# Kernel optimization log

Measured on AMD Instinct MI355X. Metric: run time of the kernel, lower is better.

The kernel has to match this reference:

```python
import jax, jax.numpy as jnp
import numpy as np

H, D_MODEL, D_K, D_V = 8, 512, 64, 64
B, S = 8, 2048


def setup_inputs() -> dict:
    key = jax.random.key(0)
    ks = jax.random.split(key, 11)
    scale = 1.0 / np.sqrt(D_MODEL)
    inp = {
        "q": jax.random.normal(ks[0], (B, S, D_MODEL), dtype=jnp.float32),
        "k": jax.random.normal(ks[1], (B, S, D_MODEL), dtype=jnp.float32),
        "v": jax.random.normal(ks[2], (B, S, D_MODEL), dtype=jnp.float32),
        # stacked per-head linear weights, [h, d_model, d_k/d_v] (in x out layout)
        "Wq": jax.random.normal(ks[3], (H, D_MODEL, D_K), dtype=jnp.float32) * scale,
        "bq": jax.random.normal(ks[4], (H, D_K), dtype=jnp.float32) * 0.01,
        "Wk": jax.random.normal(ks[5], (H, D_MODEL, D_K), dtype=jnp.float32) * scale,
        "bk": jax.random.normal(ks[6], (H, D_K), dtype=jnp.float32) * 0.01,
        "Wv": jax.random.normal(ks[7], (H, D_MODEL, D_V), dtype=jnp.float32) * scale,
        "bv": jax.random.normal(ks[8], (H, D_V), dtype=jnp.float32) * 0.01,
        "Wo": jax.random.normal(ks[9], (H * D_V, D_MODEL), dtype=jnp.float32) * (1.0 / np.sqrt(H * D_V)),
        "bo": jax.random.normal(ks[10], (D_MODEL,), dtype=jnp.float32) * 0.01,
    }
    return inp


def reference(q, k, v, Wq, bq, Wk, bk, Wv, bv, Wo, bo):
    # Per-head projections, vectorized over heads: [b, h, s, d_k]
    qh = jnp.einsum("bsd,hdk->bhsk", q, Wq) + bq[None, :, None, :]
    kh = jnp.einsum("bsd,hdk->bhsk", k, Wk) + bk[None, :, None, :]
    vh = jnp.einsum("bsd,hdv->bhsv", v, Wv) + bv[None, :, None, :]
    # scaled dot product: [b, h, s_q, s_k]
    scores = jnp.einsum("bhqd,bhkd->bhqk", qh, kh) / jnp.sqrt(jnp.float32(D_K))
    # NOTE: original applies softmax over dim=1 of [b, s_q, s_k] == the QUERY axis
    attn = jax.nn.softmax(scores, axis=2)
    ctx = jnp.einsum("bhqk,bhkv->bhqv", attn, vh)  # [b, h, s, d_v]
    # concat heads along feature dim (matches torch.cat(attentions, dim=2))
    concat = jnp.transpose(ctx, (0, 2, 1, 3)).reshape(ctx.shape[0], ctx.shape[2], H * D_V)
    return concat @ Wo + bo
```

## Files before the change

### kernel.cpp

```cpp
#include <hip/hip_runtime.h>
#include <hip/hip_bf16.h>
#include <math.h>

#define BB 8
#define SS 2048
#define HH 8
#define DM 512
#define DK 64

typedef short bf16x8 __attribute__((ext_vector_type(8)));
typedef float f32x4 __attribute__((ext_vector_type(4)));

static __device__ __forceinline__ short f2bf(float f) {
    union { __hip_bfloat16 h; short s; } u;
    u.h = __float2bfloat16(f);
    return u.s;
}

static __device__ __forceinline__ float fexp2(float x) {
#if __has_builtin(__builtin_amdgcn_exp2f)
    return __builtin_amdgcn_exp2f(x);
#else
    return __expf(x * 0.69314718056f);
#endif
}

static __device__ __forceinline__ void gld16(void* lds, const void* g) {
    __builtin_amdgcn_global_load_lds((const __attribute__((address_space(1))) void*)g,
                                     (__attribute__((address_space(3))) void*)lds, 16, 0, 0);
}

static __device__ __forceinline__ bf16x8 fragRow(const short* lds, int row, int cshort) {
    return *(const bf16x8*)(lds + row * 64 + (cshort ^ ((row & 7) << 3)));
}

static __device__ __forceinline__ void bar() {
    __builtin_amdgcn_s_barrier();
    __builtin_amdgcn_sched_barrier(0);
}
#define WAITV4 asm volatile("s_waitcnt vmcnt(4)" ::: "memory")
#define WAITV2 asm volatile("s_waitcnt vmcnt(2)" ::: "memory")
#define WAITV0 asm volatile("s_waitcnt vmcnt(0)" ::: "memory")

__global__ __launch_bounds__(256) void tcvt(const float* __restrict__ src, short* __restrict__ dst,
                                            int R, int C, int srcHS, int dstHS) {
    __shared__ short T[64][72];
    src += (size_t)blockIdx.z * srcHS;
    dst += (size_t)blockIdx.z * dstHS;
    const int r0 = blockIdx.x * 64, c0 = blockIdx.y * 64;
    const int t = threadIdx.x;
#pragma unroll
    for (int p = 0; p < 4; ++p) {
        int idx = t + 256 * p;
        int row = idx >> 4, c4 = (idx & 15) * 4;
        float4 v = *(const float4*)(src + (size_t)(r0 + row) * C + c0 + c4);
        T[c4 + 0][row] = f2bf(v.x);
        T[c4 + 1][row] = f2bf(v.y);
        T[c4 + 2][row] = f2bf(v.z);
        T[c4 + 3][row] = f2bf(v.w);
    }
    __syncthreads();
#pragma unroll
    for (int p = 0; p < 2; ++p) {
        int idx = t + 256 * p;
        int row = idx >> 3, slot = idx & 7;
        *(bf16x8*)(dst + (size_t)(c0 + row) * R + r0 + slot * 8) = *(const bf16x8*)&T[row][slot * 8];
    }
}

__global__ __launch_bounds__(256, 3) void proj_mfma(const float* __restrict__ X,
                                                    const short* __restrict__ WT,
                                                    const float* __restrict__ bias,
                                                    short* __restrict__ Y, float scale, int mode) {
    __shared__ short As[2][128 * 64];
    __shared__ short Bs[2][64 * 64];
    const int lin = blockIdx.x;
    const int b = lin & 7, h = (lin >> 3) & 7;
    const int s0 = (lin >> 6) * 128;
    const int bh = b * 8 + h;
    const int t = threadIdx.x;
    const int l = t & 63, w = t >> 6;
    const int lr = l & 15, g = l >> 4;
    const float* Xb = X + ((size_t)b * SS + s0) * DM;
    const short* Wh = WT + (size_t)h * DK * DM;
    f32x4 acc[2][4];
#pragma unroll
    for (int i = 0; i < 2; ++i)
#pragma unroll
        for (int j = 0; j < 4; ++j) acc[i][j] = (f32x4){0.f, 0.f, 0.f, 0.f};

    float4 ra[8];
    auto loadA = [&](int k0) {
#pragma unroll
        for (int p = 0; p < 4; ++p) {
            int c = p * 256 + t;
            int row = c >> 3, col = (c & 7) * 8;
            ra[2 * p]     = *(const float4*)(Xb + (size_t)row * DM + k0 + col);
            ra[2 * p + 1] = *(const float4*)(Xb + (size_t)row * DM + k0 + col + 4);
        }
    };
    auto writeA = [&](int buf) {
#pragma unroll
        for (int p = 0; p < 4; ++p) {
            int c = p * 256 + t;
            int row = c >> 3, slot = c & 7;
            bf16x8 o;
            o[0] = f2bf(ra[2 * p].x); o[1] = f2bf(ra[2 * p].y);
            o[2] = f2bf(ra[2 * p].z); o[3] = f2bf(ra[2 * p].w);
            o[4] = f2bf(ra[2 * p + 1].x); o[5] = f2bf(ra[2 * p + 1].y);
            o[6] = f2bf(ra[2 * p + 1].z); o[7] = f2bf(ra[2 * p + 1].w);
            *(bf16x8*)(As[buf] + row * 64 + ((slot ^ (row & 7)) * 8)) = o;
        }
    };
    auto stageB = [&](int buf, int k0) {
#pragma unroll
        for (int p = 0; p < 2; ++p) {
            int c = p * 256 + w * 64 + l;
            int row = c >> 3, slot = c & 7;
            gld16(Bs[buf] + (size_t)(p * 256 + w * 64) * 8,
                  Wh + (size_t)row * DM + k0 + ((slot ^ (row & 7)) * 8));
        }
    };

    loadA(0);
    stageB(0, 0);
    writeA(0);
    __syncthreads();
    int cur = 0;
    for (int k0 = 0; k0 < DM; k0 += 64) {
        const bool next = (k0 + 64 < DM);
        if (next) { loadA(k0 + 64); stageB(cur ^ 1, k0 + 64); }
        bf16x8 bfr[4][2];
#pragma unroll
        for (int bf = 0; bf < 4; ++bf) {
            bfr[bf][0] = fragRow(Bs[cur], 16 * bf + lr, 8 * g);
            bfr[bf][1] = fragRow(Bs[cur], 16 * bf + lr, 32 + 8 * g);
        }
#pragma unroll
        for (int af = 0; af < 2; ++af) {
            bf16x8 a0 = fragRow(As[cur], 32 * w + 16 * af + lr, 8 * g);
            bf16x8 a1 = fragRow(As[cur], 32 * w + 16 * af + lr, 32 + 8 * g);
#pragma unroll
            for (int bf = 0; bf < 4; ++bf) {
                acc[af][bf] = __builtin_amdgcn_mfma_f32_16x16x32_bf16(a0, bfr[bf][0], acc[af][bf], 0, 0, 0);
                acc[af][bf] = __builtin_amdgcn_mfma_f32_16x16x32_bf16(a1, bfr[bf][1], acc[af][bf], 0, 0, 0);
            }
        }
        if (next) writeA(cur ^ 1);
        __syncthreads();
        cur ^= 1;
    }
    if (mode == 2) {
        short* Yb = Y + (size_t)bh * DK * SS;
#pragma unroll
        for (int qf = 0; qf < 2; ++qf)
#pragma unroll
            for (int nf = 0; nf < 4; ++nf) {
                int n = 16 * nf + lr;
                float bv = bias[h * DK + n];
                short4 o;
                o.x = f2bf(acc[qf][nf][0] + bv);
                o.y = f2bf(acc[qf][nf][1] + bv);
                o.z = f2bf(acc[qf][nf][2] + bv);
                o.w = f2bf(acc[qf][nf][3] + bv);
                *(short4*)(Yb + (size_t)n * SS + s0 + 32 * w + 8 * g + 4 * qf) = o;
            }
    } else {
        short* Yb = Y + ((size_t)bh * SS + s0) * DK;
#pragma unroll
        for (int qf = 0; qf < 2; ++qf)
#pragma unroll
            for (int nf = 0; nf < 4; ++nf) {
                int n = 16 * nf + lr;
                float bv = bias[h * DK + n];
#pragma unroll
                for (int r = 0; r < 4; ++r)
                    Yb[(size_t)(32 * w + 16 * qf + 4 * g + r) * DK + n] =
                        f2bf((acc[qf][nf][r] + bv) * scale);
            }
    }
}

__global__ __launch_bounds__(256, 2) void stats_mfma(const short* __restrict__ qs,
                                                     const short* __restrict__ kh,
                                                     float* __restrict__ izOut) {
    __shared__ short Ks[256 * 64];
    __shared__ short Qs[3][64 * 64];
    const int bid = blockIdx.x;
    const int r = bid & 63;
    const int bh = ((r & 7) << 3) | (r >> 3);
    const int k0 = (bid >> 6) * 256;
    const int t = threadIdx.x;
    const int l = t & 63, w = t >> 6;
    const int lr = l & 15, g = l >> 4;
    const short* Qb = qs + (size_t)bh * SS * DK;
    const short* Kb = kh + ((size_t)bh * SS + k0) * DK;

#pragma unroll
    for (int p = 0; p < 8; ++p) {
        int c = p * 256 + w * 64 + l;
        int row = c >> 3, slot = c & 7;
        gld16(Ks + (size_t)(p * 256 + w * 64) * 8,
              Kb + (size_t)row * DK + ((slot ^ (row & 7)) * 8));
    }
    auto stageQ = [&](int buf, int qq) {
#pragma unroll
        for (int p = 0; p < 2; ++p) {
            int c = p * 256 + w * 64 + l;
            int row = c >> 3, slot = c & 7;
            gld16(Qs[buf] + (size_t)(p * 256 + w * 64) * 8,
                  Qb + (size_t)(qq + row) * DK + ((slot ^ (row & 7)) * 8));
        }
    };
    stageQ(0, 0);
    stageQ(1, 64);
    WAITV2;
    bar();

    bf16x8 bk[4][2];
#pragma unroll
    for (int c2 = 0; c2 < 4; ++c2) {
        bk[c2][0] = fragRow(Ks, 64 * w + 16 * c2 + lr, 8 * g);
        bk[c2][1] = fragRow(Ks, 64 * w + 16 * c2 + lr, 32 + 8 * g);
    }
    f32x4 zacc[4];
#pragma unroll
    for (int c2 = 0; c2 < 4; ++c2) zacc[c2] = (f32x4){0.f, 0.f, 0.f, 0.f};

    int cur = 0;
    for (int it = 0; it < 32; ++it) {
        const bool pre = (it < 30);
        if (pre) {
            int nb = cur + 2; if (nb >= 3) nb -= 3;
            stageQ(nb, (it + 2) * 64);
        }
#pragma unroll
        for (int qf = 0; qf < 4; ++qf) {
            bf16x8 aq0 = fragRow(Qs[cur], 16 * qf + lr, 8 * g);
            bf16x8 aq1 = fragRow(Qs[cur], 16 * qf + lr, 32 + 8 * g);
#pragma unroll
            for (int c2 = 0; c2 < 4; ++c2) {
                f32x4 s = {0.f, 0.f, 0.f, 0.f};
                s = __builtin_amdgcn_mfma_f32_16x16x32_bf16(aq0, bk[c2][0], s, 0, 0, 0);
                s = __builtin_amdgcn_mfma_f32_16x16x32_bf16(aq1, bk[c2][1], s, 0, 0, 0);
#pragma unroll
                for (int rr = 0; rr < 4; ++rr)
                    zacc[c2][rr] += fexp2(s[rr]);
            }
        }
        if (pre) { WAITV2; } else { WAITV0; }
        bar();
        cur = (cur == 2) ? 0 : cur + 1;
    }
#pragma unroll
    for (int c2 = 0; c2 < 4; ++c2) {
        float z = zacc[c2][0] + zacc[c2][1] + zacc[c2][2] + zacc[c2][3];
        z += __shfl_xor(z, 16);
        z += __shfl_xor(z, 32);
        if (l < 16)
            izOut[(size_t)bh * SS + k0 + 64 * w + 16 * c2 + l] = 1.f / z;
    }
}

__global__ __launch_bounds__(256, 2) void ctx_mfma(const short* __restrict__ qs,
                                                   const short* __restrict__ kh,
                                                   const short* __restrict__ vP,
                                                   const float* __restrict__ izArr,
                                                   short* __restrict__ ctxc) {
    __shared__ short Qs[256 * 64];
    __shared__ short Ks[3][64 * 64];
    __shared__ short Vs[3][64 * 64];
    const int bid = blockIdx.x;
    const int r = bid & 63;
    const int bh = ((r & 7) << 3) | (r >> 3);
    const int q0 = (bid >> 6) * 256;
    const int b = bh >> 3, h = bh & 7;
    const int t = threadIdx.x;
    const int l = t & 63, w = t >> 6;
    const int lr = l & 15, g = l >> 4;
    const short* Qb = qs + ((size_t)bh * SS + q0) * DK;
    const short* Kb = kh + (size_t)bh * SS * DK;
    const short* Vb = vP + (size_t)bh * DK * SS;
    const float* zB = izArr + (size_t)bh * SS;

#pragma unroll
    for (int p = 0; p < 8; ++p) {
        int c = p * 256 + w * 64 + l;
        int row = c >> 3, slot = c & 7;
        gld16(Qs + (size_t)(p * 256 + w * 64) * 8,
              Qb + (size_t)row * DK + ((slot ^ (row & 7)) * 8));
    }
    auto stageKV = [&](int buf, int kk) {
#pragma unroll
        for (int p = 0; p < 2; ++p) {
            int c = p * 256 + w * 64 + l;
            int row = c >> 3, slot = c & 7;
            gld16(Ks[buf] + (size_t)(p * 256 + w * 64) * 8,
                  Kb + (size_t)(kk + row) * DK + ((slot ^ (row & 7)) * 8));
        }
#pragma unroll
        for (int p = 0; p < 2; ++p) {
            int c = p * 256 + w * 64 + l;
            int row = c >> 3, slot = c & 7;
            gld16(Vs[buf] + (size_t)(p * 256 + w * 64) * 8,
                  Vb + (size_t)row * SS + kk + ((slot ^ (row & 7)) * 8));
        }
    };
    stageKV(0, 0);
    stageKV(1, 64);
    WAITV4;
    bar();

    bf16x8 qfr[4][2];
#pragma unroll
    for (int qf = 0; qf < 4; ++qf)
#pragma unroll
        for (int c = 0; c < 2; ++c)
            qfr[qf][c] = fragRow(Qs, 64 * w + 16 * qf + lr, 32 * c + 8 * g);

    f32x4 acc[4][4];
#pragma unroll
    for (int a = 0; a < 4; ++a)
#pragma unroll
        for (int b2 = 0; b2 < 4; ++b2) acc[a][b2] = (f32x4){0.f, 0.f, 0.f, 0.f};

    int cur = 0;
    for (int it = 0; it < 32; ++it) {
        const int k0 = it * 64;
        const bool pre = (it < 30);
        f32x4 z4[4];
#pragma unroll
        for (int kf = 0; kf < 4; ++kf)
            z4[kf] = *(const f32x4*)(zB + k0 + 16 * kf + 4 * g);
        __builtin_amdgcn_sched_barrier(0);
        if (pre) {
            int nb = cur + 2; if (nb >= 3) nb -= 3;
            stageKV(nb, k0 + 128);
        }
        bf16x8 Kf[4][2];
#pragma unroll
        for (int kf = 0; kf < 4; ++kf) {
            Kf[kf][0] = fragRow(Ks[cur], 16 * kf + lr, 8 * g);
            Kf[kf][1] = fragRow(Ks[cur], 16 * kf + lr, 32 + 8 * g);
        }
        bf16x8 pa[4][2];
#pragma unroll
        for (int qf = 0; qf < 4; ++qf) {
            float pw[4][4];
#pragma unroll
            for (int kf = 0; kf < 4; ++kf) {
                f32x4 s = {0.f, 0.f, 0.f, 0.f};
                s = __builtin_amdgcn_mfma_f32_16x16x32_bf16(Kf[kf][0], qfr[qf][0], s, 0, 0, 0);
                s = __builtin_amdgcn_mfma_f32_16x16x32_bf16(Kf[kf][1], qfr[qf][1], s, 0, 0, 0);
#pragma unroll
                for (int rr = 0; rr < 4; ++rr)
                    pw[kf][rr] = fexp2(s[rr]) * z4[kf][rr];
            }
#pragma unroll
            for (int c = 0; c < 2; ++c)
#pragma unroll
                for (int e = 0; e < 4; ++e) {
                    pa[qf][c][e]     = f2bf(pw[2 * c][e]);
                    pa[qf][c][4 + e] = f2bf(pw[2 * c + 1][e]);
                }
        }
#pragma unroll
        for (int vf = 0; vf < 4; ++vf)
#pragma unroll
            for (int c = 0; c < 2; ++c) {
                bf16x8 bv = fragRow(Vs[cur], 16 * vf + lr, 32 * c + 8 * g);
#pragma unroll
                for (int qf = 0; qf < 4; ++qf)
                    acc[qf][vf] = __builtin_amdgcn_mfma_f32_16x16x32_bf16(pa[qf][c], bv, acc[qf][vf], 0, 0, 0);
            }
        if (pre) { WAITV4; } else { WAITV0; }
        bar();
        cur = (cur == 2) ? 0 : cur + 1;
    }
    short* Cb = ctxc + ((size_t)b * SS + q0) * (HH * DK) + h * DK;
#pragma unroll
    for (int qf = 0; qf < 4; ++qf)
#pragma unroll
        for (int vf = 0; vf < 4; ++vf)
#pragma unroll
            for (int rr = 0; rr < 4; ++rr)
                Cb[(size_t)(64 * w + 16 * qf + 4 * g + rr) * (HH * DK) + 16 * vf + lr] =
                    f2bf(acc[qf][vf][rr]);
}

__global__ __launch_bounds__(256) void out_mfma(const short* __restrict__ A,
                                                const short* __restrict__ BT,
                                                const float* __restrict__ bo,
                                                float* __restrict__ out) {
    __shared__ short As[2][128 * 64];
    __shared__ short Bs[2][128 * 64];
    const int r0 = blockIdx.x * 128;
    const int j0 = blockIdx.y * 128;
    const int t = threadIdx.x;
    const int l = t & 63, w = t >> 6;
    const int lr = l & 15, g = l >> 4;
    const int wr = w >> 1, wc = w & 1;
    f32x4 acc[4][4];
#pragma unroll
    for (int i = 0; i < 4; ++i)
#pragma unroll
        for (int j = 0; j < 4; ++j) acc[i][j] = (f32x4){0.f, 0.f, 0.f, 0.f};

    auto stage = [&](int buf, int k0) {
#pragma unroll
        for (int p = 0; p < 4; ++p) {
            int c = p * 256 + w * 64 + l;
            int row = c >> 3, slot = c & 7;
            gld16(As[buf] + (size_t)(p * 256 + w * 64) * 8,
                  A + (size_t)(r0 + row) * DM + k0 + ((slot ^ (row & 7)) * 8));
            gld16(Bs[buf] + (size_t)(p * 256 + w * 64) * 8,
                  BT + (size_t)(j0 + row) * DM + k0 + ((slot ^ (row & 7)) * 8));
        }
    };
    stage(0, 0);
    WAITV0;
    __syncthreads();
    int cur = 0;
    for (int k0 = 0; k0 < DM; k0 += 64) {
        if (k0 + 64 < DM) stage(cur ^ 1, k0 + 64);
        bf16x8 bfr[4][2];
#pragma unroll
        for (int bf = 0; bf < 4; ++bf) {
            bfr[bf][0] = fragRow(Bs[cur], 64 * wc + 16 * bf + lr, 8 * g);
            bfr[bf][1] = fragRow(Bs[cur], 64 * wc + 16 * bf + lr, 32 + 8 * g);
        }
#pragma unroll
        for (int af = 0; af < 4; ++af) {
            bf16x8 a0 = fragRow(As[cur], 64 * wr + 16 * af + lr, 8 * g);
            bf16x8 a1 = fragRow(As[cur], 64 * wr + 16 * af + lr, 32 + 8 * g);
#pragma unroll
            for (int bf = 0; bf < 4; ++bf) {
                acc[af][bf] = __builtin_amdgcn_mfma_f32_16x16x32_bf16(a0, bfr[bf][0], acc[af][bf], 0, 0, 0);
                acc[af][bf] = __builtin_amdgcn_mfma_f32_16x16x32_bf16(a1, bfr[bf][1], acc[af][bf], 0, 0, 0);
            }
        }
        __syncthreads();
        cur ^= 1;
    }
#pragma unroll
    for (int af = 0; af < 4; ++af)
#pragma unroll
        for (int bf = 0; bf < 4; ++bf) {
            int j = j0 + 64 * wc + 16 * bf + lr;
            float bv = bo[j];
#pragma unroll
            for (int rr = 0; rr < 4; ++rr)
                out[(size_t)(r0 + 64 * wr + 16 * af + 4 * g + rr) * DM + j] = acc[af][bf][rr] + bv;
        }
}

extern "C" void kernel_launch(void* const* d_in, const int* in_sizes, int n_in,
                              void* d_out, int out_size, void* d_ws, size_t ws_size,
                              hipStream_t stream) {
    const float* q  = (const float*)d_in[0];
    const float* k  = (const float*)d_in[1];
    const float* v  = (const float*)d_in[2];
    const float* Wq = (const float*)d_in[3];
    const float* bq = (const float*)d_in[4];
    const float* Wk = (const float*)d_in[5];
    const float* bk = (const float*)d_in[6];
    const float* Wv = (const float*)d_in[7];
    const float* bv = (const float*)d_in[8];
    const float* Wo = (const float*)d_in[9];
    const float* bo = (const float*)d_in[10];
    float* out = (float*)d_out;

    short* w16 = (short*)d_ws;
    const size_t NH = (size_t)BB * HH * SS * DK;
    const size_t NW = (size_t)HH * DM * DK;
    short* WqT = w16;
    short* WkT = WqT + NW;
    short* WvT = WkT + NW;
    short* WoT = WvT + NW;
    short* qsb = WoT + NW;
    short* khb = qsb + NH;
    short* vtb = khb + NH;
    short* ctc = vtb + NH;
    float* izb = (float*)(ctc + NH);

    const float qscale = 0.125f * 1.4426950408889634f;

    dim3 blk(256);
    tcvt<<<dim3(8, 1, 8), blk, 0, stream>>>(Wq, WqT, DM, DK, DM * DK, DK * DM);
    tcvt<<<dim3(8, 1, 8), blk, 0, stream>>>(Wk, WkT, DM, DK, DM * DK, DK * DM);
    tcvt<<<dim3(8, 1, 8), blk, 0, stream>>>(Wv, WvT, DM, DK, DM * DK, DK * DM);
    tcvt<<<dim3(8, 8, 1), blk, 0, stream>>>(Wo, WoT, DM, DM, 0, 0);
    proj_mfma<<<dim3(1024), blk, 0, stream>>>(q, WqT, bq, qsb, qscale, 0);
    proj_mfma<<<dim3(1024), blk, 0, stream>>>(k, WkT, bk, khb, 1.0f, 1);
    proj_mfma<<<dim3(1024), blk, 0, stream>>>(v, WvT, bv, vtb, 1.0f, 2);
    stats_mfma<<<dim3(512), blk, 0, stream>>>(qsb, khb, izb);
    ctx_mfma<<<dim3(512), blk, 0, stream>>>(qsb, khb, vtb, izb, ctc);
    out_mfma<<<dim3(128, 4), blk, 0, stream>>>(ctc, WoT, bo, out);
}
```

Before: 221.6 us.

## Merge projection launches, alias LDS buffers, raise occupancy in attention kernels

The three Q/K/V weight transposes become one launch, and the three projection launches become one grid with a y-dimension selecting the mode. This cuts launch overhead and fills the device better. In stats and ctx, the resident K/Q tile is pulled into registers first, and its LDS region is then reused for the streaming buffers. This shrinks LDS use so launch bounds can rise to 4 and 3 blocks per CU. The ctx kernel also prefetches the normalizer values one iteration ahead, and both loops raise wave priority around the MFMA sections. The higher occupancy risks register pressure and spills.

```diff
diff --git a/kernel.cpp b/kernel.cpp
--- a/kernel.cpp
+++ b/kernel.cpp
@@ -41,12 +41,12 @@
 #define WAITV4 asm volatile("s_waitcnt vmcnt(4)" ::: "memory")
 #define WAITV2 asm volatile("s_waitcnt vmcnt(2)" ::: "memory")
 #define WAITV0 asm volatile("s_waitcnt vmcnt(0)" ::: "memory")
+#define WAITL0 asm volatile("s_waitcnt lgkmcnt(0)" ::: "memory")
+#define SCHED0 __builtin_amdgcn_sched_barrier(0)
 
 __global__ __launch_bounds__(256) void tcvt(const float* __restrict__ src, short* __restrict__ dst,
-                                            int R, int C, int srcHS, int dstHS) {
+                                            int R, int C) {
     __shared__ short T[64][72];
-    src += (size_t)blockIdx.z * srcHS;
-    dst += (size_t)blockIdx.z * dstHS;
     const int r0 = blockIdx.x * 64, c0 = blockIdx.y * 64;
     const int t = threadIdx.x;
 #pragma unroll
@@ -68,12 +68,57 @@
     }
 }
 
-__global__ __launch_bounds__(256, 3) void proj_mfma(const float* __restrict__ X,
-                                                    const short* __restrict__ WT,
-                                                    const float* __restrict__ bias,
-                                                    short* __restrict__ Y, float scale, int mode) {
+__global__ __launch_bounds__(256) void tcvt3(const float* __restrict__ Wq, const float* __restrict__ Wk,
+                                             const float* __restrict__ Wv, short* __restrict__ WqT,
+                                             short* __restrict__ WkT, short* __restrict__ WvT) {
+    __shared__ short T[64][72];
+    const int z = blockIdx.z;
+    const int which = z >> 3, h = z & 7;
+    const float* src = (which == 0 ? Wq : (which == 1 ? Wk : Wv)) + (size_t)h * DM * DK;
+    short* dst = (which == 0 ? WqT : (which == 1 ? WkT : WvT)) + (size_t)h * DK * DM;
+    const int r0 = blockIdx.x * 64;
+    const int t = threadIdx.x;
+#pragma unroll
+    for (int p = 0; p < 4; ++p) {
+        int idx = t + 256 * p;
+        int row = idx >> 4, c4 = (idx & 15) * 4;
+        float4 v = *(const float4*)(src + (size_t)(r0 + row) * DK + c4);
+        T[c4 + 0][row] = f2bf(v.x);
+        T[c4 + 1][row] = f2bf(v.y);
+        T[c4 + 2][row] = f2bf(v.z);
+        T[c4 + 3][row] = f2bf(v.w);
+    }
+    __syncthreads();
+#pragma unroll
+    for (int p = 0; p < 2; ++p) {
+        int idx = t + 256 * p;
+        int row = idx >> 3, slot = idx & 7;
+        *(bf16x8*)(dst + (size_t)row * DM + r0 + slot * 8) = *(const bf16x8*)&T[row][slot * 8];
+    }
+}
+
+__global__ __launch_bounds__(256, 3) void proj_mfma(const float* __restrict__ qX,
+                                                    const float* __restrict__ kX,
+                                                    const float* __restrict__ vX,
+                                                    const short* __restrict__ WqT,
+                                                    const short* __restrict__ WkT,
+                                                    const short* __restrict__ WvT,
+                                                    const float* __restrict__ bq,
+                                                    const float* __restrict__ bk,
+                                                    const float* __restrict__ bv,
+                                                    short* __restrict__ qY,
+                                                    short* __restrict__ kY,
+                                                    short* __restrict__ vY,
+                                                    float qscale) {
     __shared__ short As[2][128 * 64];
     __shared__ short Bs[2][64 * 64];
+    const int mode = blockIdx.y;
+    const float* X = mode == 0 ? qX : (mode == 1 ? kX : vX);
+    const short* WT = mode == 0 ? WqT : (mode == 1 ? WkT : WvT);
+    const float* bias = mode == 0 ? bq : (mode == 1 ? bk : bv);
+    short* Y = mode == 0 ? qY : (mode == 1 ? kY : vY);
+    const float scale = mode == 0 ? qscale : 1.0f;
+
     const int lin = blockIdx.x;
     const int b = lin & 7, h = (lin >> 3) & 7;
     const int s0 = (lin >> 6) * 128;
@@ -157,12 +202,12 @@
 #pragma unroll
             for (int nf = 0; nf < 4; ++nf) {
                 int n = 16 * nf + lr;
-                float bv = bias[h * DK + n];
+                float bv2 = bias[h * DK + n];
                 short4 o;
-                o.x = f2bf(acc[qf][nf][0] + bv);
-                o.y = f2bf(acc[qf][nf][1] + bv);
-                o.z = f2bf(acc[qf][nf][2] + bv);
-                o.w = f2bf(acc[qf][nf][3] + bv);
+                o.x = f2bf(acc[qf][nf][0] + bv2);
+                o.y = f2bf(acc[qf][nf][1] + bv2);
+                o.z = f2bf(acc[qf][nf][2] + bv2);
+                o.w = f2bf(acc[qf][nf][3] + bv2);
                 *(short4*)(Yb + (size_t)n * SS + s0 + 32 * w + 8 * g + 4 * qf) = o;
             }
     } else {
@@ -172,20 +217,19 @@
 #pragma unroll
             for (int nf = 0; nf < 4; ++nf) {
                 int n = 16 * nf + lr;
-                float bv = bias[h * DK + n];
+                float bv2 = bias[h * DK + n];
 #pragma unroll
                 for (int r = 0; r < 4; ++r)
                     Yb[(size_t)(32 * w + 16 * qf + 4 * g + r) * DK + n] =
-                        f2bf((acc[qf][nf][r] + bv) * scale);
-            }
-    }
-}
-
-__global__ __launch_bounds__(256, 2) void stats_mfma(const short* __restrict__ qs,
+                        f2bf((acc[qf][nf][r] + bv2) * scale);
+            }
+    }
+}
+
+__global__ __launch_bounds__(256, 4) void stats_mfma(const short* __restrict__ qs,
                                                      const short* __restrict__ kh,
                                                      float* __restrict__ izOut) {
-    __shared__ short Ks[256 * 64];
-    __shared__ short Qs[3][64 * 64];
+    __shared__ short LDS[16384];
     const int bid = blockIdx.x;
     const int r = bid & 63;
     const int bh = ((r & 7) << 3) | (r >> 3);
@@ -200,15 +244,27 @@
     for (int p = 0; p < 8; ++p) {
         int c = p * 256 + w * 64 + l;
         int row = c >> 3, slot = c & 7;
-        gld16(Ks + (size_t)(p * 256 + w * 64) * 8,
+        gld16(LDS + (size_t)(p * 256 + w * 64) * 8,
               Kb + (size_t)row * DK + ((slot ^ (row & 7)) * 8));
     }
+    WAITV0;
+    bar();
+    bf16x8 bk[4][2];
+#pragma unroll
+    for (int c2 = 0; c2 < 4; ++c2) {
+        bk[c2][0] = fragRow(LDS, 64 * w + 16 * c2 + lr, 8 * g);
+        bk[c2][1] = fragRow(LDS, 64 * w + 16 * c2 + lr, 32 + 8 * g);
+    }
+    WAITL0;
+    SCHED0;
+    bar();
+
     auto stageQ = [&](int buf, int qq) {
 #pragma unroll
         for (int p = 0; p < 2; ++p) {
             int c = p * 256 + w * 64 + l;
             int row = c >> 3, slot = c & 7;
-            gld16(Qs[buf] + (size_t)(p * 256 + w * 64) * 8,
+            gld16(LDS + buf * 4096 + (size_t)(p * 256 + w * 64) * 8,
                   Qb + (size_t)(qq + row) * DK + ((slot ^ (row & 7)) * 8));
         }
     };
@@ -217,12 +273,6 @@
     WAITV2;
     bar();
 
-    bf16x8 bk[4][2];
-#pragma unroll
-    for (int c2 = 0; c2 < 4; ++c2) {
-        bk[c2][0] = fragRow(Ks, 64 * w + 16 * c2 + lr, 8 * g);
-        bk[c2][1] = fragRow(Ks, 64 * w + 16 * c2 + lr, 32 + 8 * g);
-    }
     f32x4 zacc[4];
 #pragma unroll
     for (int c2 = 0; c2 < 4; ++c2) zacc[c2] = (f32x4){0.f, 0.f, 0.f, 0.f};
@@ -230,14 +280,13 @@
     int cur = 0;
     for (int it = 0; it < 32; ++it) {
         const bool pre = (it < 30);
-        if (pre) {
-            int nb = cur + 2; if (nb >= 3) nb -= 3;
-            stageQ(nb, (it + 2) * 64);
-        }
+        if (pre) stageQ((cur + 2) & 3, (it + 2) * 64);
+        const short* Qcur = LDS + cur * 4096;
+        __builtin_amdgcn_s_setprio(1);
 #pragma unroll
         for (int qf = 0; qf < 4; ++qf) {
-            bf16x8 aq0 = fragRow(Qs[cur], 16 * qf + lr, 8 * g);
-            bf16x8 aq1 = fragRow(Qs[cur], 16 * qf + lr, 32 + 8 * g);
+            bf16x8 aq0 = fragRow(Qcur, 16 * qf + lr, 8 * g);
+            bf16x8 aq1 = fragRow(Qcur, 16 * qf + lr, 32 + 8 * g);
 #pragma unroll
             for (int c2 = 0; c2 < 4; ++c2) {
                 f32x4 s = {0.f, 0.f, 0.f, 0.f};
@@ -248,9 +297,10 @@
                     zacc[c2][rr] += fexp2(s[rr]);
             }
         }
+        __builtin_amdgcn_s_setprio(0);
         if (pre) { WAITV2; } else { WAITV0; }
         bar();
-        cur = (cur == 2) ? 0 : cur + 1;
+        cur = (cur + 1) & 3;
     }
 #pragma unroll
     for (int c2 = 0; c2 < 4; ++c2) {
@@ -262,14 +312,12 @@
     }
 }
 
-__global__ __launch_bounds__(256, 2) void ctx_mfma(const short* __restrict__ qs,
+__global__ __launch_bounds__(256, 3) void ctx_mfma(const short* __restrict__ qs,
                                                    const short* __restrict__ kh,
                                                    const short* __restrict__ vP,
                                                    const float* __restrict__ izArr,
                                                    short* __restrict__ ctxc) {
-    __shared__ short Qs[256 * 64];
-    __shared__ short Ks[3][64 * 64];
-    __shared__ short Vs[3][64 * 64];
+    __shared__ short LDS[24576];
     const int bid = blockIdx.x;
     const int r = bid & 63;
     const int bh = ((r & 7) << 3) | (r >> 3);
@@ -287,36 +335,47 @@
     for (int p = 0; p < 8; ++p) {
         int c = p * 256 + w * 64 + l;
         int row = c >> 3, slot = c & 7;
-        gld16(Qs + (size_t)(p * 256 + w * 64) * 8,
+        gld16(LDS + (size_t)(p * 256 + w * 64) * 8,
               Qb + (size_t)row * DK + ((slot ^ (row & 7)) * 8));
     }
+    WAITV0;
+    bar();
+    bf16x8 qfr[4][2];
+#pragma unroll
+    for (int qf = 0; qf < 4; ++qf)
+#pragma unroll
+        for (int c = 0; c < 2; ++c)
+            qfr[qf][c] = fragRow(LDS, 64 * w + 16 * qf + lr, 32 * c + 8 * g);
+    WAITL0;
+    SCHED0;
+    bar();
+
     auto stageKV = [&](int buf, int kk) {
 #pragma unroll
         for (int p = 0; p < 2; ++p) {
             int c = p * 256 + w * 64 + l;
             int row = c >> 3, slot = c & 7;
-            gld16(Ks[buf] + (size_t)(p * 256 + w * 64) * 8,
+            gld16(LDS + buf * 4096 + (size_t)(p * 256 + w * 64) * 8,
                   Kb + (size_t)(kk + row) * DK + ((slot ^ (row & 7)) * 8));
         }
 #pragma unroll
         for (int p = 0; p < 2; ++p) {
             int c = p * 256 + w * 64 + l;
             int row = c >> 3, slot = c & 7;
-            gld16(Vs[buf] + (size_t)(p * 256 + w * 64) * 8,
+            gld16(LDS + 12288 + buf * 4096 + (size_t)(p * 256 + w * 64) * 8,
                   Vb + (size_t)row * SS + kk + ((slot ^ (row & 7)) * 8));
         }
     };
+    f32x4 zc[4], zn[4];
     stageKV(0, 0);
+    SCHED0;
+#pragma unroll
+    for (int kf = 0; kf < 4; ++kf)
+        zc[kf] = *(const f32x4*)(zB + 16 * kf + 4 * g);
+    SCHED0;
     stageKV(1, 64);
     WAITV4;
     bar();
-
-    bf16x8 qfr[4][2];
-#pragma unroll
-    for (int qf = 0; qf < 4; ++qf)
-#pragma unroll
-        for (int c = 0; c < 2; ++c)
-            qfr[qf][c] = fragRow(Qs, 64 * w + 16 * qf + lr, 32 * c + 8 * g);
 
     f32x4 acc[4][4];
 #pragma unroll
@@ -328,20 +387,24 @@
     for (int it = 0; it < 32; ++it) {
         const int k0 = it * 64;
         const bool pre = (it < 30);
-        f32x4 z4[4];
-#pragma unroll
-        for (int kf = 0; kf < 4; ++kf)
-            z4[kf] = *(const f32x4*)(zB + k0 + 16 * kf + 4 * g);
-        __builtin_amdgcn_sched_barrier(0);
+        if (it < 31) {
+#pragma unroll
+            for (int kf = 0; kf < 4; ++kf)
+                zn[kf] = *(const f32x4*)(zB + k0 + 64 + 16 * kf + 4 * g);
+        }
+        SCHED0;
         if (pre) {
             int nb = cur + 2; if (nb >= 3) nb -= 3;
             stageKV(nb, k0 + 128);
         }
+        const short* Kcur = LDS + cur * 4096;
+        const short* Vcur = LDS + 12288 + cur * 4096;
+        __builtin_amdgcn_s_setprio(1);
         bf16x8 Kf[4][2];
 #pragma unroll
         for (int kf = 0; kf < 4; ++kf) {
-            Kf[kf][0] = fragRow(Ks[cur], 16 * kf + lr, 8 * g);
-            Kf[kf][1] = fragRow(Ks[cur], 16 * kf + lr, 32 + 8 * g);
+            Kf[kf][0] = fragRow(Kcur, 16 * kf + lr, 8 * g);
+            Kf[kf][1] = fragRow(Kcur, 16 * kf + lr, 32 + 8 * g);
         }
         bf16x8 pa[4][2];
 #pragma unroll
@@ -354,7 +417,7 @@
                 s = __builtin_amdgcn_mfma_f32_16x16x32_bf16(Kf[kf][1], qfr[qf][1], s, 0, 0, 0);
 #pragma unroll
                 for (int rr = 0; rr < 4; ++rr)
-                    pw[kf][rr] = fexp2(s[rr]) * z4[kf][rr];
+                    pw[kf][rr] = fexp2(s[rr]) * zc[kf][rr];
             }
 #pragma unroll
             for (int c = 0; c < 2; ++c)
@@ -368,11 +431,14 @@
         for (int vf = 0; vf < 4; ++vf)
 #pragma unroll
             for (int c = 0; c < 2; ++c) {
-                bf16x8 bv = fragRow(Vs[cur], 16 * vf + lr, 32 * c + 8 * g);
+                bf16x8 bv2 = fragRow(Vcur, 16 * vf + lr, 32 * c + 8 * g);
 #pragma unroll
                 for (int qf = 0; qf < 4; ++qf)
-                    acc[qf][vf] = __builtin_amdgcn_mfma_f32_16x16x32_bf16(pa[qf][c], bv, acc[qf][vf], 0, 0, 0);
-            }
+                    acc[qf][vf] = __builtin_amdgcn_mfma_f32_16x16x32_bf16(pa[qf][c], bv2, acc[qf][vf], 0, 0, 0);
+            }
+        __builtin_amdgcn_s_setprio(0);
+#pragma unroll
+        for (int kf = 0; kf < 4; ++kf) zc[kf] = zn[kf];
         if (pre) { WAITV4; } else { WAITV0; }
         bar();
         cur = (cur == 2) ? 0 : cur + 1;
@@ -447,10 +513,10 @@
 #pragma unroll
         for (int bf = 0; bf < 4; ++bf) {
             int j = j0 + 64 * wc + 16 * bf + lr;
-            float bv = bo[j];
+            float bv2 = bo[j];
 #pragma unroll
             for (int rr = 0; rr < 4; ++rr)
-                out[(size_t)(r0 + 64 * wr + 16 * af + 4 * g + rr) * DM + j] = acc[af][bf][rr] + bv;
+                out[(size_t)(r0 + 64 * wr + 16 * af + 4 * g + rr) * DM + j] = acc[af][bf][rr] + bv2;
         }
 }
 
@@ -486,13 +552,10 @@
     const float qscale = 0.125f * 1.4426950408889634f;
 
     dim3 blk(256);
-    tcvt<<<dim3(8, 1, 8), blk, 0, stream>>>(Wq, WqT, DM, DK, DM * DK, DK * DM);
-    tcvt<<<dim3(8, 1, 8), blk, 0, stream>>>(Wk, WkT, DM, DK, DM * DK, DK * DM);
-    tcvt<<<dim3(8, 1, 8), blk, 0, stream>>>(Wv, WvT, DM, DK, DM * DK, DK * DM);
-    tcvt<<<dim3(8, 8, 1), blk, 0, stream>>>(Wo, WoT, DM, DM, 0, 0);
-    proj_mfma<<<dim3(1024), blk, 0, stream>>>(q, WqT, bq, qsb, qscale, 0);
-    proj_mfma<<<dim3(1024), blk, 0, stream>>>(k, WkT, bk, khb, 1.0f, 1);
-    proj_mfma<<<dim3(1024), blk, 0, stream>>>(v, WvT, bv, vtb, 1.0f, 2);
+    tcvt3<<<dim3(8, 1, 24), blk, 0, stream>>>(Wq, Wk, Wv, WqT, WkT, WvT);
+    tcvt<<<dim3(8, 8), blk, 0, stream>>>(Wo, WoT, DM, DM);
+    proj_mfma<<<dim3(1024, 3), blk, 0, stream>>>(q, k, v, WqT, WkT, WvT, bq, bk, bv,
+                                                 qsb, khb, vtb, qscale);
     stats_mfma<<<dim3(512), blk, 0, stream>>>(qsb, khb, izb);
     ctx_mfma<<<dim3(512), blk, 0, stream>>>(qsb, khb, vtb, izb, ctc);
     out_mfma<<<dim3(128, 4), blk, 0, stream>>>(ctc, WoT, bo, out);
```

New measurement: 306.7 us. 1.38x slower.
